# Kernel optimization log

Hardware: AMD Instinct MI355X
Metric: run time of the kernel (lower is better)

## Reference

```python
import jax, jax.numpy as jnp
import numpy as np

B, A, N, P, D, H = 2, 9, 1024, 4, 256, 8
DH = D // H
EPS = 1e-12


def _layernorm(x, gamma, beta):
    m = jnp.mean(x, axis=-1, keepdims=True)
    v = jnp.var(x, axis=-1, keepdims=True)
    return (x - m) / jnp.sqrt(v + EPS) * gamma + beta


def setup_inputs() -> dict:
    key = jax.random.key(0)
    ks = jax.random.split(key, 10)
    # adjacency stacks A relation matrices; scale 1/N keeps the P-step matmul chain O(1)
    adjacency = jax.random.uniform(ks[0], (B, A, N, N), jnp.float32) / N
    # diagonal, strictly positive degree matrix -> invertible
    diag = 1.0 + jax.random.uniform(ks[1], (B, N), jnp.float32)
    degree = jax.vmap(jnp.diag)(diag)
    x = jax.random.normal(ks[2], (B, N, D), jnp.float32)
    # per-head params stacked on leading H axis
    kernels = 0.1 * jax.random.normal(ks[3], (H, A, P), jnp.float32)  # RandomNormal(0, 0.1)
    lim = np.sqrt(6.0 / D).astype(np.float32)
    Wv = jax.random.uniform(ks[4], (H, D, DH), jnp.float32, -lim, lim)  # he_uniform
    Bv = jnp.zeros((H, N, DH), jnp.float32)
    W0 = jax.random.uniform(ks[5], (D, D), jnp.float32, -lim, lim)
    gamma2 = jnp.ones((D,), jnp.float32)
    beta2 = jnp.zeros((D,), jnp.float32)
    W1 = jax.random.normal(ks[6], (D, 2 * D), jnp.float32) * np.sqrt(2.0 / D).astype(np.float32)
    b1 = jnp.zeros((2 * D,), jnp.float32)
    gf = jnp.ones((2 * D,), jnp.float32)
    bf = jnp.zeros((2 * D,), jnp.float32)
    W2 = jax.random.normal(ks[7], (2 * D, D), jnp.float32) * np.sqrt(2.0 / (2 * D)).astype(np.float32)
    b2f = jnp.zeros((D,), jnp.float32)
    return {"adjacency": adjacency, "degree": degree, "x": x, "kernels": kernels,
            "Wv": Wv, "Bv": Bv, "W0": W0, "gamma2": gamma2, "beta2": beta2,
            "W1": W1, "b1": b1, "gf": gf, "bf": bf, "W2": W2, "b2f": b2f}


def reference(adjacency, degree, x, kernels, Wv, Bv, W0, gamma2, beta2, W1, b1, gf, bf, W2, b2f):
    # ---- AdjacencyAggregator (all H heads batched on leading axis) ----
    # softmax(relu(kernel)) over the input-channel (relation) axis
    soft = jax.nn.softmax(jax.nn.relu(kernels), axis=-2)  # [H, A, P]
    # 1x1 conv == per-position convex mix of the A relation matrices, one mix per path step
    # sequential chain: meta = M_0 @ M_1 @ ... @ M_{P-1}   (P is small and fixed)
    result = jnp.einsum('banm,ha->hbnm', adjacency, soft[:, :, 0])  # [H, B, N, N]
    for i in range(1, P):
        mi = jnp.einsum('banm,ha->hbnm', adjacency, soft[:, :, i])
        result = jnp.matmul(result, mi)
    inv_deg = jnp.linalg.inv(degree)                # [B, N, N], shared across heads
    normed = jnp.matmul(inv_deg[None], result)      # [H, B, N, N]
    # ---- MetaPathHead value projection + message passing ----
    V = jnp.einsum('bnd,hde->hbne', x, Wv) + Bv[:, None]   # [H, B, N, DH]
    heads = jnp.matmul(normed, V)                          # [H, B, N, DH]
    # concat along feature axis in head order
    attn = jnp.transpose(heads, (1, 2, 0, 3)).reshape(B, N, D)
    # ---- outer block: W0, residual, pre-norm FFN ----
    residual = attn @ W0 + x
    h = _layernorm(residual, gamma2, beta2)
    f = jax.nn.gelu(h @ W1 + b1, approximate=False)
    f = _layernorm(f, gf, bf)
    out = f @ W2 + b2f + residual
    return out
```

## Files before the change

### kernel.cpp

```cpp
#include <hip/hip_runtime.h>
#include <hip/hip_bf16.h>
#include <math.h>

#define B_ 2
#define A_ 9
#define N_ 1024
#define P_ 4
#define D_ 256
#define H_ 8
#define DH_ 32
#define ROWS_ (B_*N_)
#define KS_ 8
#define ADJ_ELEMS_ ((size_t)B_*A_*N_*N_)
#define SLABF4_ 131072

typedef __attribute__((ext_vector_type(8))) short bf16x8;
typedef __attribute__((ext_vector_type(4))) float f32x4;

__device__ __forceinline__ uint pack2_bf(float x, float y) {
    uint ux = __float_as_uint(x); ux += 0x7fffu + ((ux >> 16) & 1u);
    uint uy = __float_as_uint(y); uy += 0x7fffu + ((uy >> 16) & 1u);
    return (ux >> 16) | (uy & 0xffff0000u);
}
__device__ __forceinline__ float bflo(uint u){ return __uint_as_float(u << 16); }
__device__ __forceinline__ float bfhi(uint u){ return __uint_as_float(u & 0xffff0000u); }

__global__ void prep_kernel(const float* __restrict__ kernels, const float* __restrict__ degree,
                            float* __restrict__ soft, float* __restrict__ invd)
{
    int t = threadIdx.x;
    if (blockIdx.x == 0) {
        if (t < H_*P_) {
            int h = t >> 2, p = t & 3;
            float vals[A_];
            float m = 0.0f;
            #pragma unroll
            for (int a = 0; a < A_; a++) {
                float v = kernels[h*A_*P_ + a*P_ + p];
                v = v > 0.0f ? v : 0.0f;
                vals[a] = v;
                m = fmaxf(m, v);
            }
            float s = 0.0f;
            #pragma unroll
            for (int a = 0; a < A_; a++) { vals[a] = expf(vals[a] - m); s += vals[a]; }
            float inv = 1.0f / s;
            #pragma unroll
            for (int a = 0; a < A_; a++) soft[h*A_*P_ + a*P_ + p] = vals[a] * inv;
        }
    } else {
        int idx = (blockIdx.x - 1) * 256 + t;
        if (idx < ROWS_) {
            int b = idx >> 10, n = idx & (N_-1);
            invd[idx] = 1.0f / degree[(size_t)b*N_*N_ + (size_t)n*N_ + n];
        }
    }
}

__global__ void adj_pack_kernel(const float* __restrict__ in, ushort* __restrict__ out)
{
    int j = blockIdx.x * 256 + threadIdx.x;
    int kk8   = j & 3;
    int r     = (j >> 2) & 15;
    int t     = j >> 6;
    int a     = t % 9;
    int rest  = t / 9;
    int chunk = rest & 3;
    int ks    = (rest >> 2) & 7;
    int rowblk= (rest >> 5) & 63;
    int b     = rest >> 11;
    const float* src = &in[(((size_t)b*A_ + a)*N_ + (rowblk*16 + r))*N_ + ks*128 + chunk*32 + kk8*8];
    float4 v0 = *(const float4*)src;
    float4 v1 = *(const float4*)(src + 4);
    uint4 o;
    o.x = pack2_bf(v0.x, v0.y);
    o.y = pack2_bf(v0.z, v0.w);
    o.z = pack2_bf(v1.x, v1.y);
    o.w = pack2_bf(v1.z, v1.w);
    ((uint4*)out)[j] = o;
}

__global__ __launch_bounds__(256, 4)
void chain_mfma(const ushort* __restrict__ adjp, const float* __restrict__ soft,
                const ushort* __restrict__ Tin, float* __restrict__ Pp, int step)
{
    __shared__ __align__(16) ushort smem[8*640 + 16*648];
    __shared__ float soft_s[8][9];
    ushort* sm_ms = smem;
    ushort* sm_t  = smem + 8*640;

    int bid    = blockIdx.x;
    int ks     = bid & (KS_-1);
    int rowblk = (bid >> 3) & 63;
    int b      = bid >> 9;
    int n0     = rowblk * 16;
    int tid    = threadIdx.x;
    int lane   = tid & 63;
    int w      = tid >> 6;

    if (tid < 72) { int h = tid/9, a = tid%9; soft_s[h][a] = soft[h*A_*P_ + a*P_ + step]; }
    __syncthreads();

    int mr   = tid >> 4;
    int mk2  = (tid & 15) * 2;
    int mk2s = mk2 ^ ((mr & 3) << 3);
    const ushort* ablk = adjp + (size_t)((b*64 + rowblk)*8 + ks) * 18432;

    int sp  = tid >> 4;
    int sk0 = (tid & 15) * 2;
    const ushort* tbase = Tin + ((size_t)(b*16 + sp)*1024 + (size_t)ks*128) * 16;

    int g   = lane >> 4;
    int c15 = lane & 15;
    int gx  = (g ^ (c15 & 3)) * 8;

    f32x4 acc[4];
    #pragma unroll
    for (int j = 0; j < 4; j++) acc[j] = (f32x4){0.f, 0.f, 0.f, 0.f};

    for (int chunk = 0; chunk < 4; chunk++) {
        uint av[9];
        {
            const ushort* asl = ablk + chunk*4608 + mk2;
            #pragma unroll
            for (int a = 0; a < A_; a++) av[a] = *(const uint*)&asl[(a*16 + mr)*32];
        }
        const ushort* tsl = tbase + (size_t)(chunk*32 + sk0) * 16;
        uint4 q0 = *(const uint4*)(tsl + 0);
        uint4 q1 = *(const uint4*)(tsl + 8);
        uint4 q2 = *(const uint4*)(tsl + 16);
        uint4 q3 = *(const uint4*)(tsl + 24);

        if (chunk) __syncthreads();

        {
            float va0[9], va1[9];
            #pragma unroll
            for (int a = 0; a < A_; a++) { va0[a] = bflo(av[a]); va1[a] = bfhi(av[a]); }
            #pragma unroll
            for (int h = 0; h < H_; h++) {
                float s0 = soft_s[h][0]*va0[0];
                float s1 = soft_s[h][0]*va1[0];
                #pragma unroll
                for (int a = 1; a < A_; a++) { s0 += soft_s[h][a]*va0[a]; s1 += soft_s[h][a]*va1[a]; }
                *(uint*)&sm_ms[h*640 + mr*40 + mk2s] = pack2_bf(s0, s1);
            }
        }
        {
            uint l0[4] = {q0.x, q0.y, q0.z, q0.w};
            uint l1[4] = {q1.x, q1.y, q1.z, q1.w};
            uint h0[4] = {q2.x, q2.y, q2.z, q2.w};
            uint h1[4] = {q3.x, q3.y, q3.z, q3.w};
            #pragma unroll
            for (int ci = 0; ci < 8; ci++) {
                uint a0 = (l0[ci>>1] >> ((ci&1)*16)) & 0xffffu;
                uint b0 = (h0[ci>>1] >> ((ci&1)*16)) & 0xffffu;
                int k0s = sk0 ^ ((ci & 3) << 3);
                *(uint*)&sm_t[sp*648 + ci*40 + k0s] = a0 | (b0 << 16);
            }
            #pragma unroll
            for (int ci = 0; ci < 8; ci++) {
                int c = ci + 8;
                uint a0 = (l1[ci>>1] >> ((ci&1)*16)) & 0xffffu;
                uint b0 = (h1[ci>>1] >> ((ci&1)*16)) & 0xffffu;
                int k0s = sk0 ^ ((c & 3) << 3);
                *(uint*)&sm_t[sp*648 + c*40 + k0s] = a0 | (b0 << 16);
            }
        }
        __syncthreads();

        {
            const ushort* mb = sm_ms + c15*40 + gx;
            const ushort* tb = sm_t  + c15*40 + gx;
            #pragma unroll
            for (int j = 0; j < 4; j++) {
                int cg = w + 4*j;
                int h  = cg >> 1;
                bf16x8 af  = *(const bf16x8*)&mb[h*640];
                bf16x8 bfr = *(const bf16x8*)&tb[cg*648];
                acc[j] = __builtin_amdgcn_mfma_f32_16x16x32_bf16(af, bfr, acc[j], 0, 0, 0);
            }
        }
    }

    __syncthreads();
    float* Ep = (float*)smem;
    #pragma unroll
    for (int j = 0; j < 4; j++) {
        int cg = w + 4*j;
        #pragma unroll
        for (int i = 0; i < 4; i++)
            Ep[cg*256 + (g*4 + i)*16 + c15] = acc[j][i];
    }
    __syncthreads();
    {
        int p = tid >> 4, r = tid & 15;
        float* dst = Pp + (((size_t)(ks*B_ + b)*16 + p)*N_ + (n0 + r)) * 16;
        const float* src = &Ep[p*256 + r*16];
        *(float4*)&dst[0]  = *(const float4*)&src[0];
        *(float4*)&dst[4]  = *(const float4*)&src[4];
        *(float4*)&dst[8]  = *(const float4*)&src[8];
        *(float4*)&dst[12] = *(const float4*)&src[12];
    }
}

template<int FINAL>
__global__ void chain_reduce(const float* __restrict__ Pp, void* __restrict__ outp,
                             const float* __restrict__ invd)
{
    int pidx = blockIdx.x * 256 + threadIdx.x;
    float4 s = make_float4(0.f, 0.f, 0.f, 0.f);
    #pragma unroll
    for (int ks = 0; ks < KS_; ks++) {
        float4 v = ((const float4*)Pp)[(size_t)ks*SLABF4_ + pidx];
        s.x += v.x; s.y += v.y; s.z += v.z; s.w += v.w;
    }
    if constexpr (FINAL) {
        int lin = pidx * 4;
        int cc = lin & 15;
        int n  = (lin >> 4) & (N_-1);
        int cg = (lin >> 14) & 15;
        int b  = lin >> 18;
        float sc = invd[b*N_ + n];
        float4 o = make_float4(s.x*sc, s.y*sc, s.z*sc, s.w*sc);
        *(float4*)&((float*)outp)[((size_t)(b*N_ + n))*D_ + cg*16 + cc] = o;
    } else {
        uint2 wv;
        wv.x = pack2_bf(s.x, s.y);
        wv.y = pack2_bf(s.z, s.w);
        ((uint2*)outp)[pidx] = wv;
    }
}

#define BK 16
template<int MODE>
__global__ void gemm_kernel(const float* __restrict__ A, const float* __restrict__ Bm,
                            const float* __restrict__ bias, const float* __restrict__ add,
                            float* __restrict__ C, int M, int Ncols, int K)
{
    __shared__ __align__(16) float As[BK][68];
    __shared__ __align__(16) float Bs[BK][68];
    int m0 = blockIdx.x * 64;
    int n0 = blockIdx.y * 64;
    int tid = threadIdx.x;
    int tx = tid & 15, ty = tid >> 4;

    float acc[4][4];
    #pragma unroll
    for (int i = 0; i < 4; i++)
        #pragma unroll
        for (int j = 0; j < 4; j++) acc[i][j] = 0.0f;

    for (int k0 = 0; k0 < K; k0 += BK) {
        {
            int m = tid >> 2;
            int k = (tid & 3) * 4;
            float4 v = *(const float4*)&A[(size_t)(m0+m)*K + k0 + k];
            As[k+0][m] = v.x; As[k+1][m] = v.y; As[k+2][m] = v.z; As[k+3][m] = v.w;
        }
        {
            int k = tid >> 4;
            int n = (tid & 15) * 4;
            float4 v;
            if constexpr (MODE == 0) {
                int c = n0 + n; int h = c >> 5; int ee = c & 31;
                v = *(const float4*)&Bm[(size_t)h*D_*DH_ + (size_t)(k0+k)*DH_ + ee];
            } else {
                v = *(const float4*)&Bm[(size_t)(k0+k)*Ncols + n0 + n];
            }
            *(float4*)&Bs[k][n] = v;
        }
        __syncthreads();
        #pragma unroll
        for (int k = 0; k < BK; k++) {
            float4 a4 = *(const float4*)&As[k][ty*4];
            float4 b4 = *(const float4*)&Bs[k][tx*4];
            acc[0][0] += a4.x*b4.x; acc[0][1] += a4.x*b4.y; acc[0][2] += a4.x*b4.z; acc[0][3] += a4.x*b4.w;
            acc[1][0] += a4.y*b4.x; acc[1][1] += a4.y*b4.y; acc[1][2] += a4.y*b4.z; acc[1][3] += a4.y*b4.w;
            acc[2][0] += a4.z*b4.x; acc[2][1] += a4.z*b4.y; acc[2][2] += a4.z*b4.z; acc[2][3] += a4.z*b4.w;
            acc[3][0] += a4.w*b4.x; acc[3][1] += a4.w*b4.y; acc[3][2] += a4.w*b4.z; acc[3][3] += a4.w*b4.w;
        }
        __syncthreads();
    }

    #pragma unroll
    for (int i = 0; i < 4; i++) {
        int row  = m0 + ty*4 + i;
        int nloc = n0 + tx*4;
        float o[4];
        #pragma unroll
        for (int j = 0; j < 4; j++) {
            float v = acc[i][j];
            int c = nloc + j;
            if constexpr (MODE == 0) {
                int h = c >> 5, ee = c & 31, n = row & (N_-1);
                v += bias[(size_t)h*N_*DH_ + (size_t)n*DH_ + ee];
            }
            if constexpr (MODE == 1) {
                v += add[(size_t)row*Ncols + c];
            }
            if constexpr (MODE == 2) {
                v += bias[c];
                v = 0.5f * v * (1.0f + erff(v * 0.70710678118654752f));
            }
            if constexpr (MODE == 3) {
                v += bias[c] + add[(size_t)row*Ncols + c];
            }
            o[j] = v;
        }
        if constexpr (MODE == 0) {
            int bb = row >> 10, n = row & (N_-1);
            int cg = nloc >> 4, cc = nloc & 15;
            uint2 wv;
            wv.x = pack2_bf(o[0], o[1]);
            wv.y = pack2_bf(o[2], o[3]);
            *(uint2*)&((ushort*)C)[(((size_t)bb*16 + cg)*N_ + n)*16 + cc] = wv;
        } else {
            float4 ov = make_float4(o[0], o[1], o[2], o[3]);
            *(float4*)&C[(size_t)row*Ncols + nloc] = ov;
        }
    }
}

__global__ void ln_kernel(const float* __restrict__ in, float* __restrict__ out,
                          const float* __restrict__ g, const float* __restrict__ bta, int W)
{
    __shared__ float row[512];
    __shared__ float red[256];
    int r = blockIdx.x;
    int tid = threadIdx.x;
    const float* ip = in + (size_t)r * W;

    float local = 0.0f;
    for (int i = tid; i < W; i += 256) { float v = ip[i]; row[i] = v; local += v; }
    red[tid] = local;
    __syncthreads();
    for (int s = 128; s > 0; s >>= 1) {
        if (tid < s) red[tid] += red[tid + s];
        __syncthreads();
    }
    float mean = red[0] / (float)W;
    __syncthreads();

    float lv = 0.0f;
    for (int i = tid; i < W; i += 256) { float d = row[i] - mean; lv += d*d; }
    red[tid] = lv;
    __syncthreads();
    for (int s = 128; s > 0; s >>= 1) {
        if (tid < s) red[tid] += red[tid + s];
        __syncthreads();
    }
    float var = red[0] / (float)W;
    float rstd = 1.0f / sqrtf(var + 1e-12f);

    float* op = out + (size_t)r * W;
    for (int i = tid; i < W; i += 256) op[i] = (row[i] - mean) * rstd * g[i] + bta[i];
}

extern "C" void kernel_launch(void* const* d_in, const int* in_sizes, int n_in,
                              void* d_out, int out_size, void* d_ws, size_t ws_size,
                              hipStream_t stream)
{
    const float* adj    = (const float*)d_in[0];
    const float* degree = (const float*)d_in[1];
    const float* x      = (const float*)d_in[2];
    const float* kern   = (const float*)d_in[3];
    const float* Wv     = (const float*)d_in[4];
    const float* Bv     = (const float*)d_in[5];
    const float* W0     = (const float*)d_in[6];
    const float* gamma2 = (const float*)d_in[7];
    const float* beta2  = (const float*)d_in[8];
    const float* W1     = (const float*)d_in[9];
    const float* b1     = (const float*)d_in[10];
    const float* gf     = (const float*)d_in[11];
    const float* bf_    = (const float*)d_in[12];
    const float* W2     = (const float*)d_in[13];
    const float* b2f    = (const float*)d_in[14];
    float* out = (float*)d_out;
    float* ws  = (float*)d_ws;

    size_t off = 0;
    float* soft  = ws + off; off += 512;
    float* invd  = ws + off; off += 2048;
    float* T0    = ws + off; off += (size_t)ROWS_*D_;
    float* T1    = ws + off; off += (size_t)ROWS_*D_;
    float* resid = ws + off; off += (size_t)ROWS_*D_;
    float* hbuf  = ws + off; off += (size_t)ROWS_*D_;
    float* fbuf  = ws + off; off += (size_t)ROWS_*2*D_;
    float* fbuf2 = ws + off; off += (size_t)ROWS_*2*D_;
    float* Pp    = ws + off; off += (size_t)KS_*ROWS_*D_;
    ushort* adjp = (ushort*)(ws + off);

    ushort* T0b = (ushort*)T0;
    ushort* T1b = (ushort*)T1;
    float*  attn = T0;

    prep_kernel<<<9, 256, 0, stream>>>(kern, degree, soft, invd);
    adj_pack_kernel<<<(int)(ADJ_ELEMS_/8/256), 256, 0, stream>>>(adj, adjp);
    gemm_kernel<0><<<dim3(ROWS_/64, D_/64), 256, 0, stream>>>(x, Wv, Bv, nullptr, T0, ROWS_, D_, D_);
    int chain_grid  = B_*64*KS_;
    int reduce_grid = SLABF4_/256;
    chain_mfma<<<chain_grid, 256, 0, stream>>>(adjp, soft, T0b, Pp, 3);
    chain_reduce<0><<<reduce_grid, 256, 0, stream>>>(Pp, T1b, invd);
    chain_mfma<<<chain_grid, 256, 0, stream>>>(adjp, soft, T1b, Pp, 2);
    chain_reduce<0><<<reduce_grid, 256, 0, stream>>>(Pp, T0b, invd);
    chain_mfma<<<chain_grid, 256, 0, stream>>>(adjp, soft, T0b, Pp, 1);
    chain_reduce<0><<<reduce_grid, 256, 0, stream>>>(Pp, T1b, invd);
    chain_mfma<<<chain_grid, 256, 0, stream>>>(adjp, soft, T1b, Pp, 0);
    chain_reduce<1><<<reduce_grid, 256, 0, stream>>>(Pp, attn, invd);
    gemm_kernel<1><<<dim3(ROWS_/64, D_/64), 256, 0, stream>>>(attn, W0, nullptr, x, resid, ROWS_, D_, D_);
    ln_kernel<<<ROWS_, 256, 0, stream>>>(resid, hbuf, gamma2, beta2, D_);
    gemm_kernel<2><<<dim3(ROWS_/64, (2*D_)/64), 256, 0, stream>>>(hbuf, W1, b1, nullptr, fbuf, ROWS_, 2*D_, D_);
    ln_kernel<<<ROWS_, 256, 0, stream>>>(fbuf, fbuf2, gf, bf_, 2*D_);
    gemm_kernel<3><<<dim3(ROWS_/64, D_/64), 256, 0, stream>>>(fbuf2, W2, b2f, resid, out, ROWS_, D_, 2*D_);
}
```

Before: 201.5 us.

## Fuse FFN GEMMs with layernorms using bf16 MFMA full-row tiles

After: 200.5 us. No clear change (-0.5%).

```diff
diff --git a/kernel.cpp b/kernel.cpp
--- a/kernel.cpp
+++ b/kernel.cpp
@@ -205,7 +205,7 @@
 }
 
 template<int FINAL>
-__global__ void chain_reduce(const float* __restrict__ Pp, void* __restrict__ outp,
+__global__ void chain_reduce(const float* __restrict__ Pp, ushort* __restrict__ outp,
                              const float* __restrict__ invd)
 {
     int pidx = blockIdx.x * 256 + threadIdx.x;
@@ -217,26 +217,20 @@
     }
     if constexpr (FINAL) {
         int lin = pidx * 4;
-        int cc = lin & 15;
         int n  = (lin >> 4) & (N_-1);
-        int cg = (lin >> 14) & 15;
         int b  = lin >> 18;
         float sc = invd[b*N_ + n];
-        float4 o = make_float4(s.x*sc, s.y*sc, s.z*sc, s.w*sc);
-        *(float4*)&((float*)outp)[((size_t)(b*N_ + n))*D_ + cg*16 + cc] = o;
-    } else {
-        uint2 wv;
-        wv.x = pack2_bf(s.x, s.y);
-        wv.y = pack2_bf(s.z, s.w);
-        ((uint2*)outp)[pidx] = wv;
-    }
+        s.x *= sc; s.y *= sc; s.z *= sc; s.w *= sc;
+    }
+    uint2 wv;
+    wv.x = pack2_bf(s.x, s.y);
+    wv.y = pack2_bf(s.z, s.w);
+    ((uint2*)outp)[pidx] = wv;
 }
 
 #define BK 16
-template<int MODE>
-__global__ void gemm_kernel(const float* __restrict__ A, const float* __restrict__ Bm,
-                            const float* __restrict__ bias, const float* __restrict__ add,
-                            float* __restrict__ C, int M, int Ncols, int K)
+__global__ void gemm_v(const float* __restrict__ A, const float* __restrict__ Bm,
+                       const float* __restrict__ bias, ushort* __restrict__ C)
 {
     __shared__ __align__(16) float As[BK][68];
     __shared__ __align__(16) float Bs[BK][68];
@@ -251,23 +245,18 @@
         #pragma unroll
         for (int j = 0; j < 4; j++) acc[i][j] = 0.0f;
 
-    for (int k0 = 0; k0 < K; k0 += BK) {
+    for (int k0 = 0; k0 < D_; k0 += BK) {
         {
             int m = tid >> 2;
             int k = (tid & 3) * 4;
-            float4 v = *(const float4*)&A[(size_t)(m0+m)*K + k0 + k];
+            float4 v = *(const float4*)&A[(size_t)(m0+m)*D_ + k0 + k];
             As[k+0][m] = v.x; As[k+1][m] = v.y; As[k+2][m] = v.z; As[k+3][m] = v.w;
         }
         {
             int k = tid >> 4;
             int n = (tid & 15) * 4;
-            float4 v;
-            if constexpr (MODE == 0) {
-                int c = n0 + n; int h = c >> 5; int ee = c & 31;
-                v = *(const float4*)&Bm[(size_t)h*D_*DH_ + (size_t)(k0+k)*DH_ + ee];
-            } else {
-                v = *(const float4*)&Bm[(size_t)(k0+k)*Ncols + n0 + n];
-            }
+            int c = n0 + n; int h = c >> 5; int ee = c & 31;
+            float4 v = *(const float4*)&Bm[(size_t)h*D_*DH_ + (size_t)(k0+k)*DH_ + ee];
             *(float4*)&Bs[k][n] = v;
         }
         __syncthreads();
@@ -290,71 +279,335 @@
         float o[4];
         #pragma unroll
         for (int j = 0; j < 4; j++) {
-            float v = acc[i][j];
             int c = nloc + j;
-            if constexpr (MODE == 0) {
-                int h = c >> 5, ee = c & 31, n = row & (N_-1);
-                v += bias[(size_t)h*N_*DH_ + (size_t)n*DH_ + ee];
-            }
-            if constexpr (MODE == 1) {
-                v += add[(size_t)row*Ncols + c];
-            }
-            if constexpr (MODE == 2) {
-                v += bias[c];
-                v = 0.5f * v * (1.0f + erff(v * 0.70710678118654752f));
-            }
-            if constexpr (MODE == 3) {
-                v += bias[c] + add[(size_t)row*Ncols + c];
-            }
-            o[j] = v;
-        }
-        if constexpr (MODE == 0) {
-            int bb = row >> 10, n = row & (N_-1);
-            int cg = nloc >> 4, cc = nloc & 15;
-            uint2 wv;
-            wv.x = pack2_bf(o[0], o[1]);
-            wv.y = pack2_bf(o[2], o[3]);
-            *(uint2*)&((ushort*)C)[(((size_t)bb*16 + cg)*N_ + n)*16 + cc] = wv;
-        } else {
-            float4 ov = make_float4(o[0], o[1], o[2], o[3]);
-            *(float4*)&C[(size_t)row*Ncols + nloc] = ov;
-        }
-    }
-}
-
-__global__ void ln_kernel(const float* __restrict__ in, float* __restrict__ out,
-                          const float* __restrict__ g, const float* __restrict__ bta, int W)
-{
-    __shared__ float row[512];
-    __shared__ float red[256];
-    int r = blockIdx.x;
+            int h = c >> 5, ee = c & 31, n = row & (N_-1);
+            o[j] = acc[i][j] + bias[(size_t)h*N_*DH_ + (size_t)n*DH_ + ee];
+        }
+        int bb = row >> 10, n = row & (N_-1);
+        int cg = nloc >> 4, cc = nloc & 15;
+        uint2 wv;
+        wv.x = pack2_bf(o[0], o[1]);
+        wv.y = pack2_bf(o[2], o[3]);
+        *(uint2*)&C[(((size_t)bb*16 + cg)*N_ + n)*16 + cc] = wv;
+    }
+}
+
+
+__global__ __launch_bounds__(256, 2)
+void gemm_r(const ushort* __restrict__ attnp, const float* __restrict__ W0,
+            const float* __restrict__ x, const float* __restrict__ gamma,
+            const float* __restrict__ beta, float* __restrict__ resid,
+            ushort* __restrict__ hbuf)
+{
+    __shared__ __align__(16) ushort As[16*40];
+    __shared__ __align__(16) ushort Bs[256*40];
+    __shared__ float lnb[16*257];
+    __shared__ float2 stat[16];
+
+    int m0 = blockIdx.x * 16;
+    int b16 = (m0 >> 10) * 16;
+    int nb  = m0 & (N_-1);
     int tid = threadIdx.x;
-    const float* ip = in + (size_t)r * W;
-
-    float local = 0.0f;
-    for (int i = tid; i < W; i += 256) { float v = ip[i]; row[i] = v; local += v; }
-    red[tid] = local;
-    __syncthreads();
-    for (int s = 128; s > 0; s >>= 1) {
-        if (tid < s) red[tid] += red[tid + s];
+    int lane = tid & 63;
+    int w = tid >> 6;
+    int g = lane >> 4, c15 = lane & 15;
+    int gx = (g ^ (c15 & 3)) * 8;
+
+    int am = tid >> 4, ak2 = (tid & 15) * 2;
+    int apos = am*40 + ((((ak2>>3) ^ (am&3))) << 3) + (ak2 & 7);
+    int bn8 = (tid & 31) * 8;
+    int bkq = (tid >> 5) * 4;
+    int bpos0 = (((bkq>>3)) << 3) + (bkq & 7);
+
+    f32x4 acc[4];
+    #pragma unroll
+    for (int j = 0; j < 4; j++) acc[j] = (f32x4){0.f,0.f,0.f,0.f};
+
+    for (int ks = 0; ks < 8; ks++) {
+        int k0 = ks * 32;
+        int k = k0 + ak2;
+        uint av = *(const uint*)&attnp[(((size_t)(b16 + (k>>4)))*N_ + nb + am)*16 + (k & 15)];
+        float4 lo[4], hi[4];
+        #pragma unroll
+        for (int i = 0; i < 4; i++) {
+            lo[i] = *(const float4*)&W0[(size_t)(k0+bkq+i)*D_ + bn8];
+            hi[i] = *(const float4*)&W0[(size_t)(k0+bkq+i)*D_ + bn8 + 4];
+        }
+        if (ks) __syncthreads();
+        *(uint*)&As[apos] = av;
+        #pragma unroll
+        for (int jn = 0; jn < 8; jn++) {
+            int n = bn8 + jn;
+            float v0 = (jn<4)? ((const float*)&lo[0])[jn] : ((const float*)&hi[0])[jn-4];
+            float v1 = (jn<4)? ((const float*)&lo[1])[jn] : ((const float*)&hi[1])[jn-4];
+            float v2 = (jn<4)? ((const float*)&lo[2])[jn] : ((const float*)&hi[2])[jn-4];
+            float v3 = (jn<4)? ((const float*)&lo[3])[jn] : ((const float*)&hi[3])[jn-4];
+            uint2 wv; wv.x = pack2_bf(v0, v1); wv.y = pack2_bf(v2, v3);
+            *(uint2*)&Bs[n*40 + (bpos0 ^ ((n&3)<<3))] = wv;
+        }
         __syncthreads();
-    }
-    float mean = red[0] / (float)W;
-    __syncthreads();
-
-    float lv = 0.0f;
-    for (int i = tid; i < W; i += 256) { float d = row[i] - mean; lv += d*d; }
-    red[tid] = lv;
-    __syncthreads();
-    for (int s = 128; s > 0; s >>= 1) {
-        if (tid < s) red[tid] += red[tid + s];
+        const ushort* ab = As + c15*40 + gx;
+        #pragma unroll
+        for (int nt = 0; nt < 4; nt++) {
+            int n = w*64 + nt*16 + c15;
+            bf16x8 af  = *(const bf16x8*)ab;
+            bf16x8 bfr = *(const bf16x8*)&Bs[n*40 + gx];
+            acc[nt] = __builtin_amdgcn_mfma_f32_16x16x32_bf16(af, bfr, acc[nt], 0, 0, 0);
+        }
+    }
+    __syncthreads();
+
+    #pragma unroll
+    for (int nt = 0; nt < 4; nt++) {
+        int c = w*64 + nt*16 + c15;
+        #pragma unroll
+        for (int i = 0; i < 4; i++) {
+            int r = g*4 + i;
+            lnb[r*257 + c] = acc[nt][i] + x[(size_t)(m0+r)*D_ + c];
+        }
+    }
+    __syncthreads();
+
+    {
+        int rr = tid >> 4, sl = tid & 15;
+        float sum = 0.f, sq = 0.f;
+        #pragma unroll
+        for (int j = 0; j < 16; j++) {
+            float v = lnb[rr*257 + sl + 16*j];
+            sum += v; sq += v*v;
+        }
+        #pragma unroll
+        for (int m = 1; m < 16; m <<= 1) { sum += __shfl_xor(sum, m); sq += __shfl_xor(sq, m); }
+        if (sl == 0) {
+            float mean = sum * (1.0f/D_);
+            float var  = fmaxf(sq * (1.0f/D_) - mean*mean, 0.f);
+            stat[rr] = make_float2(mean, rsqrtf(var + 1e-12f));
+        }
+    }
+    __syncthreads();
+
+    {
+        int rr = tid & 15, s2 = tid >> 4;
+        float2 ms = stat[rr];
+        int c0 = s2 * 16;
+        uint hw[8];
+        #pragma unroll
+        for (int q = 0; q < 4; q++) {
+            int c = c0 + q*4;
+            float4 v = *(const float4*)&lnb[rr*257 + c];
+            *(float4*)&resid[(size_t)(m0+rr)*D_ + c] = v;
+            float4 gm = *(const float4*)&gamma[c];
+            float4 bt = *(const float4*)&beta[c];
+            float h0 = (v.x - ms.x)*ms.y*gm.x + bt.x;
+            float h1 = (v.y - ms.x)*ms.y*gm.y + bt.y;
+            float h2 = (v.z - ms.x)*ms.y*gm.z + bt.z;
+            float h3 = (v.w - ms.x)*ms.y*gm.w + bt.w;
+            hw[2*q]   = pack2_bf(h0, h1);
+            hw[2*q+1] = pack2_bf(h2, h3);
+        }
+        ushort* hp = &hbuf[(size_t)(m0+rr)*D_ + c0];
+        *(uint4*)&hp[0] = make_uint4(hw[0], hw[1], hw[2], hw[3]);
+        *(uint4*)&hp[8] = make_uint4(hw[4], hw[5], hw[6], hw[7]);
+    }
+}
+
+__global__ __launch_bounds__(256, 2)
+void gemm_f1(const ushort* __restrict__ hbuf, const float* __restrict__ W1,
+             const float* __restrict__ b1, const float* __restrict__ gf,
+             const float* __restrict__ bfv, ushort* __restrict__ fout)
+{
+    __shared__ __align__(16) ushort As[16*40];
+    __shared__ __align__(16) ushort Bs[512*40];
+    __shared__ float lnb[16*513];
+    __shared__ float2 stat[16];
+
+    int m0 = blockIdx.x * 16;
+    int tid = threadIdx.x;
+    int lane = tid & 63;
+    int w = tid >> 6;
+    int g = lane >> 4, c15 = lane & 15;
+    int gx = (g ^ (c15 & 3)) * 8;
+
+    int am = tid >> 4, ak2 = (tid & 15) * 2;
+    int apos = am*40 + ((((ak2>>3) ^ (am&3))) << 3) + (ak2 & 7);
+    int bn8 = (tid & 63) * 8;
+    int bk8 = (tid >> 6) * 8;
+
+    f32x4 acc[8];
+    #pragma unroll
+    for (int j = 0; j < 8; j++) acc[j] = (f32x4){0.f,0.f,0.f,0.f};
+
+    for (int ks = 0; ks < 8; ks++) {
+        int k0 = ks * 32;
+        uint av = *(const uint*)&hbuf[(size_t)(m0+am)*D_ + k0 + ak2];
+        float4 q[16];
+        #pragma unroll
+        for (int i = 0; i < 8; i++) {
+            q[2*i]   = *(const float4*)&W1[(size_t)(k0+bk8+i)*(2*D_) + bn8];
+            q[2*i+1] = *(const float4*)&W1[(size_t)(k0+bk8+i)*(2*D_) + bn8 + 4];
+        }
+        if (ks) __syncthreads();
+        *(uint*)&As[apos] = av;
+        #pragma unroll
+        for (int jn = 0; jn < 8; jn++) {
+            int n = bn8 + jn;
+            float e0 = (jn<4)? ((const float*)&q[0])[jn]  : ((const float*)&q[1])[jn-4];
+            float e1 = (jn<4)? ((const float*)&q[2])[jn]  : ((const float*)&q[3])[jn-4];
+            float e2 = (jn<4)? ((const float*)&q[4])[jn]  : ((const float*)&q[5])[jn-4];
+            float e3 = (jn<4)? ((const float*)&q[6])[jn]  : ((const float*)&q[7])[jn-4];
+            float e4 = (jn<4)? ((const float*)&q[8])[jn]  : ((const float*)&q[9])[jn-4];
+            float e5 = (jn<4)? ((const float*)&q[10])[jn] : ((const float*)&q[11])[jn-4];
+            float e6 = (jn<4)? ((const float*)&q[12])[jn] : ((const float*)&q[13])[jn-4];
+            float e7 = (jn<4)? ((const float*)&q[14])[jn] : ((const float*)&q[15])[jn-4];
+            uint4 wv;
+            wv.x = pack2_bf(e0, e1); wv.y = pack2_bf(e2, e3);
+            wv.z = pack2_bf(e4, e5); wv.w = pack2_bf(e6, e7);
+            *(uint4*)&Bs[n*40 + ((((bk8>>3) ^ (n&3))) << 3)] = wv;
+        }
         __syncthreads();
-    }
-    float var = red[0] / (float)W;
-    float rstd = 1.0f / sqrtf(var + 1e-12f);
-
-    float* op = out + (size_t)r * W;
-    for (int i = tid; i < W; i += 256) op[i] = (row[i] - mean) * rstd * g[i] + bta[i];
+        const ushort* ab = As + c15*40 + gx;
+        #pragma unroll
+        for (int nt = 0; nt < 8; nt++) {
+            int n = w*128 + nt*16 + c15;
+            bf16x8 af  = *(const bf16x8*)ab;
+            bf16x8 bfr = *(const bf16x8*)&Bs[n*40 + gx];
+            acc[nt] = __builtin_amdgcn_mfma_f32_16x16x32_bf16(af, bfr, acc[nt], 0, 0, 0);
+        }
+    }
+    __syncthreads();
+
+    #pragma unroll
+    for (int nt = 0; nt < 8; nt++) {
+        int c = w*128 + nt*16 + c15;
+        float bias = b1[c];
+        #pragma unroll
+        for (int i = 0; i < 4; i++) {
+            int r = g*4 + i;
+            float v = acc[nt][i] + bias;
+            v = 0.5f * v * (1.0f + erff(v * 0.70710678118654752f));
+            lnb[r*513 + c] = v;
+        }
+    }
+    __syncthreads();
+
+    {
+        int rr = tid >> 4, sl = tid & 15;
+        float sum = 0.f, sq = 0.f;
+        #pragma unroll
+        for (int j = 0; j < 32; j++) {
+            float v = lnb[rr*513 + sl + 16*j];
+            sum += v; sq += v*v;
+        }
+        #pragma unroll
+        for (int m = 1; m < 16; m <<= 1) { sum += __shfl_xor(sum, m); sq += __shfl_xor(sq, m); }
+        if (sl == 0) {
+            float mean = sum * (1.0f/(2*D_));
+            float var  = fmaxf(sq * (1.0f/(2*D_)) - mean*mean, 0.f);
+            stat[rr] = make_float2(mean, rsqrtf(var + 1e-12f));
+        }
+    }
+    __syncthreads();
+
+    {
+        int rr = tid & 15, s2 = tid >> 4;
+        float2 ms = stat[rr];
+        int c0 = s2 * 32;
+        #pragma unroll
+        for (int q = 0; q < 8; q++) {
+            int c = c0 + q*4;
+            float4 v = *(const float4*)&lnb[rr*513 + c];
+            float4 gm = *(const float4*)&gf[c];
+            float4 bt = *(const float4*)&bfv[c];
+            float h0 = (v.x - ms.x)*ms.y*gm.x + bt.x;
+            float h1 = (v.y - ms.x)*ms.y*gm.y + bt.y;
+            float h2 = (v.z - ms.x)*ms.y*gm.z + bt.z;
+            float h3 = (v.w - ms.x)*ms.y*gm.w + bt.w;
+            *(uint2*)&fout[(size_t)(m0+rr)*(2*D_) + c] = make_uint2(pack2_bf(h0,h1), pack2_bf(h2,h3));
+        }
+    }
+}
+
+__global__ __launch_bounds__(256, 2)
+void gemm_f2(const ushort* __restrict__ fbuf, const float* __restrict__ W2,
+             const float* __restrict__ b2f, const float* __restrict__ resid,
+             float* __restrict__ outp)
+{
+    __shared__ __align__(16) ushort As[16*40];
+    __shared__ __align__(16) ushort Bs[256*40];
+    __shared__ float lnb[16*257];
+
+    int m0 = blockIdx.x * 16;
+    int tid = threadIdx.x;
+    int lane = tid & 63;
+    int w = tid >> 6;
+    int g = lane >> 4, c15 = lane & 15;
+    int gx = (g ^ (c15 & 3)) * 8;
+
+    int am = tid >> 4, ak2 = (tid & 15) * 2;
+    int apos = am*40 + ((((ak2>>3) ^ (am&3))) << 3) + (ak2 & 7);
+    int bn8 = (tid & 31) * 8;
+    int bkq = (tid >> 5) * 4;
+    int bpos0 = (((bkq>>3)) << 3) + (bkq & 7);
+
+    f32x4 acc[4];
+    #pragma unroll
+    for (int j = 0; j < 4; j++) acc[j] = (f32x4){0.f,0.f,0.f,0.f};
+
+    for (int ks = 0; ks < 16; ks++) {
+        int k0 = ks * 32;
+        uint av = *(const uint*)&fbuf[(size_t)(m0+am)*(2*D_) + k0 + ak2];
+        float4 lo[4], hi[4];
+        #pragma unroll
+        for (int i = 0; i < 4; i++) {
+            lo[i] = *(const float4*)&W2[(size_t)(k0+bkq+i)*D_ + bn8];
+            hi[i] = *(const float4*)&W2[(size_t)(k0+bkq+i)*D_ + bn8 + 4];
+        }
+        if (ks) __syncthreads();
+        *(uint*)&As[apos] = av;
+        #pragma unroll
+        for (int jn = 0; jn < 8; jn++) {
+            int n = bn8 + jn;
+            float v0 = (jn<4)? ((const float*)&lo[0])[jn] : ((const float*)&hi[0])[jn-4];
+            float v1 = (jn<4)? ((const float*)&lo[1])[jn] : ((const float*)&hi[1])[jn-4];
+            float v2 = (jn<4)? ((const float*)&lo[2])[jn] : ((const float*)&hi[2])[jn-4];
+            float v3 = (jn<4)? ((const float*)&lo[3])[jn] : ((const float*)&hi[3])[jn-4];
+            uint2 wv; wv.x = pack2_bf(v0, v1); wv.y = pack2_bf(v2, v3);
+            *(uint2*)&Bs[n*40 + (bpos0 ^ ((n&3)<<3))] = wv;
+        }
+        __syncthreads();
+        const ushort* ab = As + c15*40 + gx;
+        #pragma unroll
+        for (int nt = 0; nt < 4; nt++) {
+            int n = w*64 + nt*16 + c15;
+            bf16x8 af  = *(const bf16x8*)ab;
+            bf16x8 bfr = *(const bf16x8*)&Bs[n*40 + gx];
+            acc[nt] = __builtin_amdgcn_mfma_f32_16x16x32_bf16(af, bfr, acc[nt], 0, 0, 0);
+        }
+    }
+    __syncthreads();
+
+    #pragma unroll
+    for (int nt = 0; nt < 4; nt++) {
+        int c = w*64 + nt*16 + c15;
+        #pragma unroll
+        for (int i = 0; i < 4; i++)
+            lnb[(g*4+i)*257 + c] = acc[nt][i];
+    }
+    __syncthreads();
+
+    {
+        int rr = tid & 15, s2 = tid >> 4;
+        int c0 = s2 * 16;
+        #pragma unroll
+        for (int q = 0; q < 4; q++) {
+            int c = c0 + q*4;
+            float4 v  = *(const float4*)&lnb[rr*257 + c];
+            float4 bb = *(const float4*)&b2f[c];
+            float4 rs = *(const float4*)&resid[(size_t)(m0+rr)*D_ + c];
+            float4 o = make_float4(v.x+bb.x+rs.x, v.y+bb.y+rs.y, v.z+bb.z+rs.z, v.w+bb.w+rs.w);
+            *(float4*)&outp[(size_t)(m0+rr)*D_ + c] = o;
+        }
+    }
 }
 
 extern "C" void kernel_launch(void* const* d_in, const int* in_sizes, int n_in,
@@ -390,14 +643,17 @@
     float* fbuf2 = ws + off; off += (size_t)ROWS_*2*D_;
     float* Pp    = ws + off; off += (size_t)KS_*ROWS_*D_;
     ushort* adjp = (ushort*)(ws + off);
+    (void)fbuf2;
 
     ushort* T0b = (ushort*)T0;
     ushort* T1b = (ushort*)T1;
-    float*  attn = T0;
+    ushort* hb  = (ushort*)hbuf;
+    ushort* fb  = (ushort*)fbuf;
 
     prep_kernel<<<9, 256, 0, stream>>>(kern, degree, soft, invd);
     adj_pack_kernel<<<(int)(ADJ_ELEMS_/8/256), 256, 0, stream>>>(adj, adjp);
-    gemm_kernel<0><<<dim3(ROWS_/64, D_/64), 256, 0, stream>>>(x, Wv, Bv, nullptr, T0, ROWS_, D_, D_);
+    gemm_v<<<dim3(ROWS_/64, D_/64), 256, 0, stream>>>(x, Wv, Bv, T0b);
+
     int chain_grid  = B_*64*KS_;
     int reduce_grid = SLABF4_/256;
     chain_mfma<<<chain_grid, 256, 0, stream>>>(adjp, soft, T0b, Pp, 3);
@@ -407,10 +663,9 @@
     chain_mfma<<<chain_grid, 256, 0, stream>>>(adjp, soft, T0b, Pp, 1);
     chain_reduce<0><<<reduce_grid, 256, 0, stream>>>(Pp, T1b, invd);
     chain_mfma<<<chain_grid, 256, 0, stream>>>(adjp, soft, T1b, Pp, 0);
-    chain_reduce<1><<<reduce_grid, 256, 0, stream>>>(Pp, attn, invd);
-    gemm_kernel<1><<<dim3(ROWS_/64, D_/64), 256, 0, stream>>>(attn, W0, nullptr, x, resid, ROWS_, D_, D_);
-    ln_kernel<<<ROWS_, 256, 0, stream>>>(resid, hbuf, gamma2, beta2, D_);
-    gemm_kernel<2><<<dim3(ROWS_/64, (2*D_)/64), 256, 0, stream>>>(hbuf, W1, b1, nullptr, fbuf, ROWS_, 2*D_, D_);
-    ln_kernel<<<ROWS_, 256, 0, stream>>>(fbuf, fbuf2, gf, bf_, 2*D_);
-    gemm_kernel<3><<<dim3(ROWS_/64, D_/64), 256, 0, stream>>>(fbuf2, W2, b2f, resid, out, ROWS_, D_, 2*D_);
-}
+    chain_reduce<1><<<reduce_grid, 256, 0, stream>>>(Pp, T0b, invd);
+
+    gemm_r <<<ROWS_/16, 256, 0, stream>>>(T0b, W0, x, gamma2, beta2, resid, hb);
+    gemm_f1<<<ROWS_/16, 256, 0, stream>>>(hb, W1, b1, gf, bf_, fb);
+    gemm_f2<<<ROWS_/16, 256, 0, stream>>>(fb, W2, b2f, resid, out);
+}
```
